# Optimization experiments

Measured on AMD Instinct MI355X. Metric: run time of the kernel, lower is better.

## Reference

```python
import jax, jax.numpy as jnp
import numpy as np

P = 0.8
XINT_MAX = 0.125; ROT_MAX = 10.0
BRI_STD = 0.2; CON_STD = 0.2; HUE_MAX = 0.95; SAT_STD = 0.2; SHARP_STD = 1.0; NOISE_STD = 0.1

def _gate(key, B, p):
    k1, k2 = jax.random.split(key)
    bern = jax.random.randint(k1, (B,), 0, 2).astype(jnp.float32)
    u = jax.random.uniform(k2, ())
    return bern * p > u  # [B] bool, matches randint(0,2)*flag*p > random()

def _sel(m, new, old):
    return jnp.where(m[:, None, None, None], new, old)

def _warp(imgs, angle_deg, tx, ty, nearest=False):
    # inverse-affine resample: rotate by angle (deg, CCW) about center, then translate (tx,ty) px; zero fill
    B, C, H, W = imgs.shape
    th = jnp.deg2rad(jnp.asarray(angle_deg, jnp.float32))
    c, s = jnp.cos(th), jnp.sin(th)
    cy, cx = (H - 1) / 2.0, (W - 1) / 2.0
    ys, xs = jnp.meshgrid(jnp.arange(H, dtype=jnp.float32), jnp.arange(W, dtype=jnp.float32), indexing='ij')
    dx = xs - cx - tx; dy = ys - cy - ty
    sx = c * dx + s * dy + cx
    sy = -s * dx + c * dy + cy
    if nearest:
        xi = jnp.round(sx); yi = jnp.round(sy)
        valid = (xi >= 0) & (xi < W) & (yi >= 0) & (yi < H)
        xc = jnp.clip(xi, 0, W - 1).astype(jnp.int32)
        yc = jnp.clip(yi, 0, H - 1).astype(jnp.int32)
        return imgs[:, :, yc, xc] * valid
    x0 = jnp.floor(sx); y0 = jnp.floor(sy)
    wx = sx - x0; wy = sy - y0
    def g(yi, xi):
        valid = (xi >= 0) & (xi < W) & (yi >= 0) & (yi < H)
        yc = jnp.clip(yi, 0, H - 1).astype(jnp.int32)
        xc = jnp.clip(xi, 0, W - 1).astype(jnp.int32)
        return imgs[:, :, yc, xc] * valid
    v00 = g(y0, x0); v01 = g(y0, x0 + 1); v10 = g(y0 + 1, x0); v11 = g(y0 + 1, x0 + 1)
    top = v00 * (1 - wx) + v01 * wx
    bot = v10 * (1 - wx) + v11 * wx
    return top * (1 - wy) + bot * wy

def _gray(x):
    return 0.2989 * x[:, 0:1] + 0.587 * x[:, 1:2] + 0.114 * x[:, 2:3]

def _blend(a, b, ratio):
    return jnp.clip(ratio * a + (1.0 - ratio) * b, 0.0, 1.0)

def _rgb_to_hsv(x):
    r, g, b = x[:, 0], x[:, 1], x[:, 2]
    maxc = jnp.maximum(jnp.maximum(r, g), b)
    minc = jnp.minimum(jnp.minimum(r, g), b)
    cr = maxc - minc
    s = cr / jnp.where(maxc == 0, 1.0, maxc)
    crd = jnp.where(cr == 0, 1.0, cr)
    rc = (maxc - r) / crd; gc = (maxc - g) / crd; bc = (maxc - b) / crd
    h = jnp.where(maxc == r, bc - gc, jnp.where(maxc == g, 2.0 + rc - bc, 4.0 + gc - rc))
    h = jnp.where(cr == 0, 0.0, (h / 6.0) % 1.0)
    return jnp.stack([h, s, maxc], axis=1)

def _hsv_to_rgb(x):
    h, s, v = x[:, 0], x[:, 1], x[:, 2]
    i = jnp.floor(h * 6.0)
    f = h * 6.0 - i
    p = v * (1 - s); q = v * (1 - f * s); t = v * (1 - (1 - f) * s)
    ii = i.astype(jnp.int32) % 6
    conds = [ii == 0, ii == 1, ii == 2, ii == 3, ii == 4, ii == 5]
    r = jnp.select(conds, [v, q, p, p, t, v])
    g = jnp.select(conds, [t, v, v, q, p, p])
    b = jnp.select(conds, [p, p, t, v, v, q])
    return jnp.stack([r, g, b], axis=1)

def _sharp_degenerate(x):
    C, H, W = x.shape[1], x.shape[2], x.shape[3]
    k = jnp.array([[1., 1., 1.], [1., 5., 1.], [1., 1., 1.]], jnp.float32) / 13.0
    w = jnp.tile(k[None, None], (C, 1, 1, 1))
    blur = jax.lax.conv_general_dilated(x, w, (1, 1), 'SAME', feature_group_count=C,
                                        dimension_numbers=('NCHW', 'OIHW', 'NCHW'))
    blur = jnp.clip(blur, 0.0, 1.0)
    interior = jnp.zeros((H, W), bool).at[1:-1, 1:-1].set(True)
    return jnp.where(interior, blur, x)  # torchvision keeps original border pixels

def _augment(images, masks):
    key = jax.random.key(42)
    ks = jax.random.split(key, 18)
    B = images.shape[0]
    img = (images + 1.0) * 0.5
    msk = masks
    # xflip
    m = _gate(ks[0], B, P)
    img = _sel(m, img[:, :, :, ::-1], img)
    msk = _sel(m, msk[:, :, :, ::-1], msk)
    # rotate90 (square images: exact)
    m = _gate(ks[1], B, P)
    img = _sel(m, jnp.rot90(img, 1, axes=(2, 3)), img)
    msk = _sel(m, jnp.rot90(msk, 1, axes=(2, 3)), msk)
    # xint translation
    m = _gate(ks[2], B, P)
    t = jax.random.uniform(ks[3], ()) * XINT_MAX
    img = _sel(m, _warp(img, 0.0, t, t), img)
    msk = _sel(m, _warp(msk, 0.0, t, t, nearest=True), msk)
    # rotate
    m = _gate(ks[4], B, P)
    r = jax.random.uniform(ks[5], ()) * ROT_MAX
    img = _sel(m, _warp(img, r, 0.0, 0.0), img)
    msk = _sel(m, _warp(msk, r, 0.0, 0.0, nearest=True), msk)
    # hue
    m = _gate(ks[6], B, P)
    h = (jax.random.uniform(ks[7], ()) - 0.5) * HUE_MAX
    hsv = _rgb_to_hsv(jnp.clip(img, 0.0, 1.0))
    hsv = hsv.at[:, 0].set((hsv[:, 0] + h) % 1.0)
    img = _sel(m, _hsv_to_rgb(hsv), img)
    # brightness
    m = _gate(ks[8], B, P)
    b = jnp.abs(1.0 + jax.random.normal(ks[9], ()) * BRI_STD)
    img = _sel(m, jnp.clip(img * b, 0.0, 1.0), img)
    # contrast
    m = _gate(ks[10], B, P)
    c = jnp.abs(1.0 + jax.random.normal(ks[11], ()) * CON_STD)
    mean = _gray(img).mean(axis=(2, 3), keepdims=True)
    img = _sel(m, _blend(img, mean, c), img)
    # saturation
    m = _gate(ks[12], B, P)
    s = jnp.abs(1.0 + jax.random.normal(ks[13], ()) * SAT_STD)
    img = _sel(m, _blend(img, _gray(img), s), img)
    # sharpness (bug-faithful: std == self.sharpness == 1.0)
    m = _gate(ks[14], B, P)
    sh = jnp.abs(1.0 + jax.random.normal(ks[15], ()) * SHARP_STD)
    img = _sel(m, _blend(img, _sharp_degenerate(img), sh), img)
    # noise
    m = _gate(ks[16], B, P)
    n = jax.random.normal(ks[17], img.shape, img.dtype) * NOISE_STD
    img = _sel(m, img + n, img)
    img = (img - 0.5) / 0.5
    return img, msk

def setup_inputs() -> dict:
    key = jax.random.key(0)
    k1, k2 = jax.random.split(key)
    images = jax.random.uniform(k1, (32, 3, 512, 512), jnp.float32, -1.0, 1.0)
    masks = (jax.random.uniform(k2, (32, 1, 512, 512), jnp.float32) > 0.5).astype(jnp.float32)
    return {"images": images, "masks": masks}

def reference(images, masks):
    return _augment(images, masks)
```

## Files before the change

### kernel.cpp

```cpp
#include <hip/hip_runtime.h>
#include <stdint.h>
#include <math.h>

#define HH 512
#define WW 512
#define BB 32
#define CC 3
#define HWSZ (HH*WW)
#define CHW (CC*HWSZ)
#define NIMG (BB*CHW)
#define NMSK (BB*HWSZ)

__host__ __device__ inline uint32_t rotl32(uint32_t x, uint32_t r){ return (x<<r)|(x>>(32u-r)); }

__host__ __device__ inline void tf2x32(uint32_t k0, uint32_t k1, uint32_t x0, uint32_t x1,
                                       uint32_t& o0, uint32_t& o1){
  uint32_t kx = k0 ^ k1 ^ 0x1BD11BDAu;
  uint32_t ks[3] = {k0, k1, kx};
  const uint32_t R[2][4] = {{13u,15u,26u,6u},{17u,29u,16u,24u}};
  x0 += ks[0]; x1 += ks[1];
  #pragma unroll
  for (int i = 0; i < 5; ++i){
    #pragma unroll
    for (int j = 0; j < 4; ++j){
      x0 += x1; x1 = rotl32(x1, R[i & 1][j]); x1 ^= x0;
    }
    x0 += ks[(i+1)%3];
    x1 += ks[(i+2)%3] + (uint32_t)(i+1);
  }
  o0 = x0; o1 = x1;
}

__host__ __device__ inline float bits_to_u01(uint32_t b){
  uint32_t fb = (b >> 9) | 0x3f800000u;
  float f;
#ifdef __HIP_DEVICE_COMPILE__
  f = __uint_as_float(fb);
#else
  union { uint32_t u; float f; } cv; cv.u = fb; f = cv.f;
#endif
  return f - 1.0f;
}

__host__ __device__ inline float erfinv_f32(float x){
  float w = -log1pf(-x*x);
  float p;
  if (w < 5.0f){
    w -= 2.5f;
    p = 2.81022636e-08f;
    p = fmaf(p, w, 3.43273939e-07f);
    p = fmaf(p, w, -3.5233877e-06f);
    p = fmaf(p, w, -4.39150654e-06f);
    p = fmaf(p, w, 0.00021858087f);
    p = fmaf(p, w, -0.00125372503f);
    p = fmaf(p, w, -0.00417768164f);
    p = fmaf(p, w, 0.246640727f);
    p = fmaf(p, w, 1.50140941f);
  } else {
    w = sqrtf(w) - 3.0f;
    p = -0.000200214257f;
    p = fmaf(p, w, 0.000100950558f);
    p = fmaf(p, w, 0.00134934322f);
    p = fmaf(p, w, -0.00367342844f);
    p = fmaf(p, w, 0.00573950773f);
    p = fmaf(p, w, -0.0076224613f);
    p = fmaf(p, w, 0.00943887047f);
    p = fmaf(p, w, 1.00167406f);
    p = fmaf(p, w, 2.83297682f);
  }
  return p * x;
}

#define NRM_LO (-0.9999999403953552f)
#define SQRT2F 1.41421356237309504880f

__host__ __device__ inline float normal_from_bits(uint32_t b){
  float f = bits_to_u01(b);
  float val = f * 2.0f + NRM_LO;
  val = fmaxf(NRM_LO, val);
  return SQRT2F * erfinv_f32(val);
}

struct Key { uint32_t a, b; };

static Key foldSplit(Key k, uint32_t j){
  Key r; tf2x32(k.a, k.b, 0u, j, r.a, r.b); return r;
}

static uint32_t bits32(Key k, uint32_t i){
  uint32_t o0, o1; tf2x32(k.a, k.b, 0u, i, o0, o1); return o0 ^ o1;
}

static float unif_scalar(Key k){ return bits_to_u01(bits32(k, 0u)); }
static float normal_scalar(Key k){ return normal_from_bits(bits32(k, 0u)); }

static uint32_t gate_mask(Key kg){
  Key k1 = foldSplit(kg, 0u);
  Key k2 = foldSplit(kg, 1u);
  Key kl = foldSplit(k1, 1u);
  float u = bits_to_u01(bits32(k2, 0u));
  uint32_t m = 0;
  for (uint32_t i = 0; i < 32; ++i){
    float bern = (float)(bits32(kl, i) & 1u);
    if (bern * 0.8f > u) m |= (1u << i);
  }
  return m;
}

struct AugParams {
  uint32_t mFlip, mRot90, mTrans, mRot, mHue, mBri, mCon, mSat, mSharp, mNoise;
  float t, rotC, rotS, hShift, bri, con, sat, shp;
  uint32_t nk0, nk1;
};

__device__ inline float clip01(float v){ return fminf(fmaxf(v, 0.0f), 1.0f); }

__device__ inline void permIdx(int y, int x, bool r9, bool fl, int& py, int& px){
  if (r9){ py = x; px = 511 - y; } else { py = y; px = x; }
  if (fl) px = 511 - px;
}

__device__ inline float tapP(const float* __restrict__ src, int y, int x, bool r9, bool fl){
  if ((unsigned)x >= 512u || (unsigned)y >= 512u) return 0.0f;
  int py, px; permIdx(y, x, r9, fl, py, px);
  return (src[py*512 + px] + 1.0f) * 0.5f;
}

__device__ inline void stage1RGB(const float* __restrict__ base, int ty, int tx,
                                 bool r9, bool fl, bool tr, float t, float out[3]){
  if (!tr){
    #pragma unroll
    for (int c = 0; c < 3; ++c) out[c] = tapP(base + c*HWSZ, ty, tx, r9, fl);
    return;
  }
  float sx = (((float)tx - 255.5f) - t) + 255.5f;
  float sy = (((float)ty - 255.5f) - t) + 255.5f;
  float x0f = floorf(sx), y0f = floorf(sy);
  float wx = sx - x0f, wy = sy - y0f;
  int x0 = (int)x0f, y0 = (int)y0f;
  #pragma unroll
  for (int c = 0; c < 3; ++c){
    const float* s = base + c*HWSZ;
    float v00 = tapP(s, y0,   x0,   r9, fl);
    float v01 = tapP(s, y0,   x0+1, r9, fl);
    float v10 = tapP(s, y0+1, x0,   r9, fl);
    float v11 = tapP(s, y0+1, x0+1, r9, fl);
    float top = v00*(1.0f-wx) + v01*wx;
    float bot = v10*(1.0f-wx) + v11*wx;
    out[c] = top*(1.0f-wy) + bot*wy;
  }
}

__device__ inline void rotTap(const float* __restrict__ base, int ty, int tx,
                              bool r9, bool fl, bool tr, float t, float o[3]){
  if ((unsigned)tx < 512u && (unsigned)ty < 512u){
    stage1RGB(base, ty, tx, r9, fl, tr, t, o);
  } else {
    o[0] = o[1] = o[2] = 0.0f;
  }
}

__device__ inline void rgb2hsv(float r, float g, float b, float& h, float& s, float& v){
  float maxc = fmaxf(fmaxf(r, g), b);
  float minc = fminf(fminf(r, g), b);
  float cr = maxc - minc;
  s = cr / ((maxc == 0.0f) ? 1.0f : maxc);
  float crd = (cr == 0.0f) ? 1.0f : cr;
  float rc = (maxc - r) / crd;
  float gc = (maxc - g) / crd;
  float bc = (maxc - b) / crd;
  float hh;
  if (maxc == r)      hh = bc - gc;
  else if (maxc == g) hh = 2.0f + rc - bc;
  else                hh = 4.0f + gc - rc;
  if (cr == 0.0f) hh = 0.0f;
  else { hh = hh / 6.0f; hh = hh - floorf(hh); }
  h = hh; v = maxc;
}

__device__ inline void hsv2rgb(float h, float s, float v, float& r, float& g, float& b){
  float i = floorf(h * 6.0f);
  float f = h * 6.0f - i;
  float p = v * (1.0f - s);
  float q = v * (1.0f - f * s);
  float t = v * (1.0f - (1.0f - f) * s);
  int ii = ((int)i) % 6;
  switch (ii){
    case 0: r = v; g = t; b = p; break;
    case 1: r = q; g = v; b = p; break;
    case 2: r = p; g = v; b = t; break;
    case 3: r = p; g = q; b = v; break;
    case 4: r = t; g = p; b = v; break;
    default: r = v; g = p; b = q; break;
  }
}

__device__ inline void applyHB(float v[3], bool hue, bool bri, const AugParams& P){
  if (hue){
    float r = clip01(v[0]), g = clip01(v[1]), bb = clip01(v[2]);
    float h, s, val;
    rgb2hsv(r, g, bb, h, s, val);
    h = h + P.hShift;
    h = h - floorf(h);
    hsv2rgb(h, s, val, v[0], v[1], v[2]);
  }
  if (bri){
    #pragma unroll
    for (int c = 0; c < 3; ++c) v[c] = clip01(v[c] * P.bri);
  }
}

__device__ inline void stage2RGB(const float* __restrict__ base, int yy, int xx,
                                 const AugParams& P, int b, float v[3]){
  bool fl  = (P.mFlip  >> b) & 1u;
  bool r9  = (P.mRot90 >> b) & 1u;
  bool tr  = (P.mTrans >> b) & 1u;
  bool rot = (P.mRot   >> b) & 1u;
  if (rot){
    float dx = (float)xx - 255.5f;
    float dy = (float)yy - 255.5f;
    float sx = (P.rotC*dx + P.rotS*dy) + 255.5f;
    float sy = (-P.rotS*dx + P.rotC*dy) + 255.5f;
    float x0f = floorf(sx), y0f = floorf(sy);
    float wx = sx - x0f, wy = sy - y0f;
    int x0 = (int)x0f, y0 = (int)y0f;
    float q00[3], q01[3], q10[3], q11[3];
    rotTap(base, y0,   x0,   r9, fl, tr, P.t, q00);
    rotTap(base, y0,   x0+1, r9, fl, tr, P.t, q01);
    rotTap(base, y0+1, x0,   r9, fl, tr, P.t, q10);
    rotTap(base, y0+1, x0+1, r9, fl, tr, P.t, q11);
    #pragma unroll
    for (int c = 0; c < 3; ++c){
      float top = q00[c]*(1.0f-wx) + q01[c]*wx;
      float bot = q10[c]*(1.0f-wx) + q11[c]*wx;
      v[c] = top*(1.0f-wy) + bot*wy;
    }
  } else {
    stage1RGB(base, yy, xx, r9, fl, tr, P.t, v);
  }
  applyHB(v, (P.mHue >> b) & 1u, (P.mBri >> b) & 1u, P);
}

__device__ inline float s1at(const float* __restrict__ s, int y, int x){
  return ((unsigned)x < 512u && (unsigned)y < 512u) ? s[y*512 + x] : 0.0f;
}

__device__ inline void stage2S1(const float* __restrict__ s1b, int yy, int xx,
                                const AugParams& P, int b, float v[3]){
  bool rot = (P.mRot >> b) & 1u;
  bool hue = (P.mHue >> b) & 1u;
  bool bri = (P.mBri >> b) & 1u;
  if (rot){
    float dx = (float)xx - 255.5f;
    float dy = (float)yy - 255.5f;
    float sx = (P.rotC*dx + P.rotS*dy) + 255.5f;
    float sy = (-P.rotS*dx + P.rotC*dy) + 255.5f;
    float x0f = floorf(sx), y0f = floorf(sy);
    float wx = sx - x0f, wy = sy - y0f;
    int x0 = (int)x0f, y0 = (int)y0f;
    #pragma unroll
    for (int c = 0; c < 3; ++c){
      const float* s = s1b + c*HWSZ;
      float v00 = s1at(s, y0,   x0);
      float v01 = s1at(s, y0,   x0+1);
      float v10 = s1at(s, y0+1, x0);
      float v11 = s1at(s, y0+1, x0+1);
      float top = v00*(1.0f-wx) + v01*wx;
      float bot = v10*(1.0f-wx) + v11*wx;
      v[c] = top*(1.0f-wy) + bot*wy;
    }
  } else {
    #pragma unroll
    for (int c = 0; c < 3; ++c) v[c] = s1b[c*HWSZ + yy*512 + xx];
  }
  applyHB(v, hue, bri, P);
}

__device__ inline void procCS(float v[3], bool con, float cmul, float cadd, bool sat, float smul){
  if (con){
    #pragma unroll
    for (int c = 0; c < 3; ++c) v[c] = clip01(cmul * v[c] + cadd);
  }
  if (sat){
    float g = 0.2989f*v[0] + 0.587f*v[1] + 0.114f*v[2];
    float gadd = (1.0f - smul) * g;
    #pragma unroll
    for (int c = 0; c < 3; ++c) v[c] = clip01(smul * v[c] + gadd);
  }
}


__global__ void kZero(float* meanAcc){
  int t = threadIdx.x;
  if (t < 32) meanAcc[t] = 0.0f;
}


__global__ __launch_bounds__(256) void kStage1(const float* __restrict__ img,
                                               float* __restrict__ S1,
                                               float* __restrict__ meanAcc, AugParams P){
  __shared__ float ptile[3][33][33];
  __shared__ float wsum[4];
  int b = blockIdx.z;
  bool fl  = (P.mFlip  >> b) & 1u;
  bool r9  = (P.mRot90 >> b) & 1u;
  bool tr  = (P.mTrans >> b) & 1u;
  bool rot = (P.mRot   >> b) & 1u;
  bool con = (P.mCon   >> b) & 1u;
  bool hue = (P.mHue   >> b) & 1u;
  bool bri = (P.mBri   >> b) & 1u;
  bool accM = con && !rot;
  int X0 = blockIdx.x*32, Y0 = blockIdx.y*32;
  int tx = threadIdx.x, ty = threadIdx.y;
  int tid = ty*32 + tx;
  const float* base = img + (size_t)b*CHW;
  float* dstb = S1 + (size_t)b*CHW;
  float t = P.t;
  float gsum = 0.0f;

  if (!r9 && !tr){
    #pragma unroll
    for (int k = 0; k < 4; ++k){
      int y = Y0 + ty + 8*k, x = X0 + tx;
      int px = fl ? (511 - x) : x;
      float v[3];
      #pragma unroll
      for (int c = 0; c < 3; ++c){
        v[c] = (base[c*HWSZ + y*512 + px] + 1.0f) * 0.5f;
        dstb[(size_t)c*HWSZ + (size_t)y*512 + x] = v[c];
      }
      if (accM){
        float w[3] = {v[0], v[1], v[2]};
        applyHB(w, hue, bri, P);
        gsum += 0.2989f*w[0] + 0.587f*w[1] + 0.114f*w[2];
      }
    }
  } else if (!r9){
    #pragma unroll
    for (int k = 0; k < 4; ++k){
      int y = Y0 + ty + 8*k, x = X0 + tx;
      float v[3];
      stage1RGB(base, y, x, false, fl, true, t, v);
      #pragma unroll
      for (int c = 0; c < 3; ++c)
        dstb[(size_t)c*HWSZ + (size_t)y*512 + x] = v[c];
      if (accM){
        float w[3] = {v[0], v[1], v[2]};
        applyHB(w, hue, bri, P);
        gsum += 0.2989f*w[0] + 0.587f*w[1] + 0.114f*w[2];
      }
    }
  } else {
    #pragma unroll
    for (int c = 0; c < 3; ++c){
      const float* src = base + c*HWSZ;
      for (int idx = tid; idx < 33*33; idx += 256){
        int r = idx / 33, q = idx - r*33;
        int xx = X0 - 1 + r;
        int yy = Y0 - 1 + q;
        float val = 0.0f;
        if ((unsigned)yy < 512u && (unsigned)xx < 512u){
          int col = fl ? yy : (511 - yy);
          val = (src[xx*512 + col] + 1.0f) * 0.5f;
        }
        ptile[c][q][r] = val;
      }
    }
    __syncthreads();
    #pragma unroll
    for (int k = 0; k < 4; ++k){
      int y = Y0 + ty + 8*k, x = X0 + tx;
      float v[3];
      if (tr){
        float sx = (((float)x - 255.5f) - t) + 255.5f;
        float sy = (((float)y - 255.5f) - t) + 255.5f;
        float x0f = floorf(sx), y0f = floorf(sy);
        float wx = sx - x0f, wy = sy - y0f;
        int lx0 = (int)x0f - (X0 - 1);
        int ly0 = (int)y0f - (Y0 - 1);
        #pragma unroll
        for (int c = 0; c < 3; ++c){
          float v00 = ptile[c][ly0][lx0],   v01 = ptile[c][ly0][lx0+1];
          float v10 = ptile[c][ly0+1][lx0], v11 = ptile[c][ly0+1][lx0+1];
          float top = v00*(1.0f-wx) + v01*wx;
          float bot = v10*(1.0f-wx) + v11*wx;
          v[c] = top*(1.0f-wy) + bot*wy;
        }
      } else {
        #pragma unroll
        for (int c = 0; c < 3; ++c) v[c] = ptile[c][ty+8*k+1][tx+1];
      }
      #pragma unroll
      for (int c = 0; c < 3; ++c)
        dstb[(size_t)c*HWSZ + (size_t)y*512 + x] = v[c];
      if (accM){
        float w[3] = {v[0], v[1], v[2]};
        applyHB(w, hue, bri, P);
        gsum += 0.2989f*w[0] + 0.587f*w[1] + 0.114f*w[2];
      }
    }
  }

  if (accM){
    #pragma unroll
    for (int off = 32; off > 0; off >>= 1) gsum += __shfl_down(gsum, off);
    int wid = tid >> 6, lid = tid & 63;
    if (lid == 0) wsum[wid] = gsum;
    __syncthreads();
    if (tid == 0) atomicAdd(&meanAcc[b], wsum[0] + wsum[1] + wsum[2] + wsum[3]);
  }
}

__global__ __launch_bounds__(256) void kMaskStage(const float* __restrict__ msk,
                                                  float* __restrict__ M1,
                                                  float* __restrict__ outMsk, AugParams P){
  __shared__ float mtile[32][33];
  int b = blockIdx.z;
  bool fl  = (P.mFlip  >> b) & 1u;
  bool r9  = (P.mRot90 >> b) & 1u;
  bool rot = (P.mRot   >> b) & 1u;
  int X0 = blockIdx.x*32, Y0 = blockIdx.y*32;
  int tx = threadIdx.x, ty = threadIdx.y;
  int tid = ty*32 + tx;
  const float* src = msk + (size_t)b*HWSZ;
  float* dst = (rot ? M1 : outMsk) + (size_t)b*HWSZ;
  if (!r9){
    #pragma unroll
    for (int k = 0; k < 4; ++k){
      int y = Y0 + ty + 8*k, x = X0 + tx;
      int px = fl ? (511 - x) : x;
      dst[y*512 + x] = src[y*512 + px];
    }
  } else {
    for (int idx = tid; idx < 32*32; idx += 256){
      int r = idx >> 5, q = idx & 31;
      int xx = X0 + r;
      int yy = Y0 + q;
      int col = fl ? yy : (511 - yy);
      mtile[q][r] = src[xx*512 + col];
    }
    __syncthreads();
    #pragma unroll
    for (int k = 0; k < 4; ++k){
      int y = Y0 + ty + 8*k, x = X0 + tx;
      dst[y*512 + x] = mtile[ty + 8*k][tx];
    }
  }
}

__global__ __launch_bounds__(256) void kMaskRot(const float* __restrict__ M1,
                                                float* __restrict__ outMsk, AugParams P){
  int b = blockIdx.z;
  if (!((P.mRot >> b) & 1u)) return;
  int X0 = blockIdx.x*32, Y0 = blockIdx.y*32;
  int tx = threadIdx.x, ty = threadIdx.y;
  const float* src = M1 + (size_t)b*HWSZ;
  float* dst = outMsk + (size_t)b*HWSZ;
  #pragma unroll
  for (int k = 0; k < 4; ++k){
    int x = X0 + tx, y = Y0 + ty + 8*k;
    float dx = __fsub_rn((float)x, 255.5f);
    float dy = __fsub_rn((float)y, 255.5f);
    float sx = __fadd_rn(__fadd_rn(__fmul_rn(P.rotC, dx), __fmul_rn(P.rotS, dy)), 255.5f);
    float sy = __fadd_rn(__fadd_rn(__fmul_rn(-P.rotS, dx), __fmul_rn(P.rotC, dy)), 255.5f);
    float xi = rintf(sx), yi = rintf(sy);
    bool valid = (xi >= 0.0f) && (xi < 512.0f) && (yi >= 0.0f) && (yi < 512.0f);
    int xc = (int)fminf(fmaxf(xi, 0.0f), 511.0f);
    int yc = (int)fminf(fmaxf(yi, 0.0f), 511.0f);
    float v = valid ? src[yc*512 + xc] : 0.0f;
    dst[y*512 + x] = v;
  }
}

__global__ __launch_bounds__(256) void kMean2(const float* __restrict__ S1,
                                              float* __restrict__ meanAcc, AugParams P){
  int b = blockIdx.z;
  if (!((P.mCon >> b) & 1u) || !((P.mRot >> b) & 1u)) return;
  int tid = threadIdx.x;
  const float* base = S1 + (size_t)b*CHW;
  int pbase = blockIdx.x * 4096;
  float lsum = 0.0f;

  #pragma unroll 4
  for (int j = 0; j < 16; ++j){
    int px = pbase + j*256 + tid;
    int y = px >> 9, x = px & 511;
    float v[3];
    stage2S1(base, y, x, P, b, v);
    lsum += 0.2989f*v[0] + 0.587f*v[1] + 0.114f*v[2];
  }

  #pragma unroll
  for (int off = 32; off > 0; off >>= 1) lsum += __shfl_down(lsum, off);
  __shared__ float wsum[4];
  int wid = tid >> 6, lid = tid & 63;
  if (lid == 0) wsum[wid] = lsum;
  __syncthreads();
  if (tid == 0) atomicAdd(&meanAcc[b], wsum[0] + wsum[1] + wsum[2] + wsum[3]);
}

__global__ __launch_bounds__(256) void kFinal2(const float* __restrict__ S1,
                                               const float* __restrict__ meanAcc,
                                               float* __restrict__ out, AugParams P){
  __shared__ float s2[34][34][3];
  int tx = threadIdx.x, ty = threadIdx.y;
  int tid = ty*32 + tx;
  int bx = blockIdx.x, by = blockIdx.y, b = blockIdx.z;
  const float W1 = 1.0f/13.0f, W5 = 5.0f/13.0f;

  bool con = (P.mCon   >> b) & 1u;
  bool sat = (P.mSat   >> b) & 1u;
  bool shg = (P.mSharp >> b) & 1u;
  bool noi = (P.mNoise >> b) & 1u;
  float mean = meanAcc[b] * (1.0f/262144.0f);
  float cadd = (1.0f - P.con) * mean;
  const float* base = S1 + (size_t)b*CHW;

  if (!shg){
    #pragma unroll
    for (int k = 0; k < 4; ++k){
      int x = bx*32 + tx, y = by*32 + ty + 8*k;
      float res[3];
      stage2S1(base, y, x, P, b, res);
      procCS(res, con, P.con, cadd, sat, P.sat);
      if (noi){
        #pragma unroll
        for (int c = 0; c < 3; ++c){
          uint32_t idx = (uint32_t)(b*CHW + c*HWSZ + y*512 + x);
          uint32_t o0, o1;
          tf2x32(P.nk0, P.nk1, 0u, idx, o0, o1);
          res[c] += normal_from_bits(o0 ^ o1) * 0.1f;
        }
      }
      #pragma unroll
      for (int c = 0; c < 3; ++c){
        out[(size_t)b*CHW + (size_t)c*HWSZ + (size_t)y*512 + x] = (res[c] - 0.5f) * 2.0f;
      }
    }
    return;
  }

  for (int cell = tid; cell < 34*34; cell += 256){
    int r = cell / 34, cc = cell - r*34;
    int gy = by*32 + r - 1, gx = bx*32 + cc - 1;
    float v[3] = {0.0f, 0.0f, 0.0f};
    if ((unsigned)gx < 512u && (unsigned)gy < 512u){
      stage2S1(base, gy, gx, P, b, v);
      procCS(v, con, P.con, cadd, sat, P.sat);
    }
    s2[r][cc][0] = v[0]; s2[r][cc][1] = v[1]; s2[r][cc][2] = v[2];
  }
  __syncthreads();

  for (int k = 0; k < 4; ++k){
    int yy = ty + 8*k;
    int x = bx*32 + tx, y = by*32 + yy;
    bool interior = (x >= 1) && (x <= 510) && (y >= 1) && (y <= 510);
    float res[3];
    float c0[3] = { s2[yy+1][tx+1][0], s2[yy+1][tx+1][1], s2[yy+1][tx+1][2] };
    if (interior){
      float nsum[3] = {0.0f, 0.0f, 0.0f};
      #pragma unroll
      for (int dy = 0; dy < 3; ++dy){
        #pragma unroll
        for (int dxx = 0; dxx < 3; ++dxx){
          if (dxx == 1 && dy == 1) continue;
          #pragma unroll
          for (int c = 0; c < 3; ++c) nsum[c] += s2[yy+dy][tx+dxx][c];
        }
      }
      #pragma unroll
      for (int c = 0; c < 3; ++c){
        float bl = clip01(nsum[c]*W1 + c0[c]*W5);
        res[c] = clip01(P.shp * c0[c] + (1.0f - P.shp) * bl);
      }
    } else {
      res[0] = c0[0]; res[1] = c0[1]; res[2] = c0[2];
    }

    if (noi){
      #pragma unroll
      for (int c = 0; c < 3; ++c){
        uint32_t idx = (uint32_t)(b*CHW + c*HWSZ + y*512 + x);
        uint32_t o0, o1;
        tf2x32(P.nk0, P.nk1, 0u, idx, o0, o1);
        res[c] += normal_from_bits(o0 ^ o1) * 0.1f;
      }
    }
    #pragma unroll
    for (int c = 0; c < 3; ++c){
      out[(size_t)b*CHW + (size_t)c*HWSZ + (size_t)y*512 + x] = (res[c] - 0.5f) * 2.0f;
    }
  }
}


__global__ __launch_bounds__(256) void kMask(const float* __restrict__ msk,
                                             float* __restrict__ out, AugParams P){
  int x = blockIdx.x*blockDim.x + threadIdx.x;
  int y = blockIdx.y*blockDim.y + threadIdx.y;
  int b = blockIdx.z;
  bool fl  = (P.mFlip  >> b) & 1u;
  bool r9  = (P.mRot90 >> b) & 1u;
  bool rot = (P.mRot   >> b) & 1u;
  float v;
  if (rot){
    float dx = __fsub_rn((float)x, 255.5f);
    float dy = __fsub_rn((float)y, 255.5f);
    float sx = __fadd_rn(__fadd_rn(__fmul_rn(P.rotC, dx), __fmul_rn(P.rotS, dy)), 255.5f);
    float sy = __fadd_rn(__fadd_rn(__fmul_rn(-P.rotS, dx), __fmul_rn(P.rotC, dy)), 255.5f);
    float xi = rintf(sx), yi = rintf(sy);
    bool valid = (xi >= 0.0f) && (xi < 512.0f) && (yi >= 0.0f) && (yi < 512.0f);
    int xc = (int)fminf(fmaxf(xi, 0.0f), 511.0f);
    int yc = (int)fminf(fmaxf(yi, 0.0f), 511.0f);
    int py, px; permIdx(yc, xc, r9, fl, py, px);
    v = valid ? msk[(size_t)b*HWSZ + py*512 + px] : 0.0f;
  } else {
    int py, px; permIdx(y, x, r9, fl, py, px);
    v = msk[(size_t)b*HWSZ + py*512 + px];
  }
  out[(size_t)b*HWSZ + y*512 + x] = v;
}

__global__ __launch_bounds__(256) void kMean(const float* __restrict__ img,
                                             float* __restrict__ meanAcc, AugParams P){
  int b = blockIdx.z;
  if (!((P.mCon >> b) & 1u)) return;
  int x = blockIdx.x*blockDim.x + threadIdx.x;
  int y = blockIdx.y*blockDim.y + threadIdx.y;
  float v[3];
  stage2RGB(img + (size_t)b*CHW, y, x, P, b, v);
  float gray = 0.2989f*v[0] + 0.587f*v[1] + 0.114f*v[2];
  __shared__ float sred[256];
  int tid = threadIdx.y*blockDim.x + threadIdx.x;
  sred[tid] = gray;
  __syncthreads();
  for (int s = 128; s > 0; s >>= 1){
    if (tid < s) sred[tid] += sred[tid + s];
    __syncthreads();
  }
  if (tid == 0) atomicAdd(&meanAcc[b], sred[0]);
}

__global__ __launch_bounds__(256) void kFinal(const float* __restrict__ img,
                                              const float* __restrict__ meanAcc,
                                              float* __restrict__ out, AugParams P){
  __shared__ float s2[10][34][3];
  int tx = threadIdx.x, ty = threadIdx.y;
  int tid = ty*32 + tx;
  int bx = blockIdx.x, by = blockIdx.y, b = blockIdx.z;
  const float W1 = 1.0f/13.0f, W5 = 5.0f/13.0f;

  bool con = (P.mCon   >> b) & 1u;
  bool sat = (P.mSat   >> b) & 1u;
  bool shg = (P.mSharp >> b) & 1u;
  bool noi = (P.mNoise >> b) & 1u;
  float mean = meanAcc[b] * (1.0f/262144.0f);
  float cadd = (1.0f - P.con) * mean;
  const float* base = img + (size_t)b*CHW;

  for (int cell = tid; cell < 340; cell += 256){
    int r = cell / 34, cc = cell % 34;
    int gy = by*8 + r - 1, gx = bx*32 + cc - 1;
    float v[3] = {0.0f, 0.0f, 0.0f};
    if ((unsigned)gx < 512u && (unsigned)gy < 512u){
      stage2RGB(base, gy, gx, P, b, v);
      procCS(v, con, P.con, cadd, sat, P.sat);
    }
    s2[r][cc][0] = v[0]; s2[r][cc][1] = v[1]; s2[r][cc][2] = v[2];
  }
  __syncthreads();

  int x = bx*32 + tx, y = by*8 + ty;
  bool interior = (x >= 1) && (x <= 510) && (y >= 1) && (y <= 510);
  float res[3];
  float c0[3] = { s2[ty+1][tx+1][0], s2[ty+1][tx+1][1], s2[ty+1][tx+1][2] };
  if (shg && interior){
    float nsum[3] = {0.0f, 0.0f, 0.0f};
    #pragma unroll
    for (int dy = 0; dy < 3; ++dy){
      #pragma unroll
      for (int dxx = 0; dxx < 3; ++dxx){
        if (dxx == 1 && dy == 1) continue;
        #pragma unroll
        for (int c = 0; c < 3; ++c) nsum[c] += s2[ty+dy][tx+dxx][c];
      }
    }
    #pragma unroll
    for (int c = 0; c < 3; ++c){
      float bl = clip01(nsum[c]*W1 + c0[c]*W5);
      res[c] = clip01(P.shp * c0[c] + (1.0f - P.shp) * bl);
    }
  } else {
    res[0] = c0[0]; res[1] = c0[1]; res[2] = c0[2];
  }

  if (noi){
    #pragma unroll
    for (int c = 0; c < 3; ++c){
      uint32_t idx = (uint32_t)(b*CHW + c*HWSZ + y*512 + x);
      uint32_t o0, o1;
      tf2x32(P.nk0, P.nk1, 0u, idx, o0, o1);
      res[c] += normal_from_bits(o0 ^ o1) * 0.1f;
    }
  }
  #pragma unroll
  for (int c = 0; c < 3; ++c){
    out[(size_t)b*CHW + (size_t)c*HWSZ + y*512 + x] = (res[c] - 0.5f) * 2.0f;
  }
}

extern "C" void kernel_launch(void* const* d_in, const int* in_sizes, int n_in,
                              void* d_out, int out_size, void* d_ws, size_t ws_size,
                              hipStream_t stream) {
  (void)in_sizes; (void)n_in; (void)out_size;
  const float* images = (const float*)d_in[0];
  const float* masks  = (const float*)d_in[1];
  float* out_img = (float*)d_out;
  float* out_msk = out_img + (size_t)NIMG;
  float* meanAcc = (float*)d_ws;

  Key root; root.a = 0u; root.b = 42u;
  Key ks[18];
  for (uint32_t j = 0; j < 18; ++j) ks[j] = foldSplit(root, j);

  AugParams P;
  P.mFlip  = gate_mask(ks[0]);
  P.mRot90 = gate_mask(ks[1]);
  P.mTrans = gate_mask(ks[2]);
  P.t      = unif_scalar(ks[3]) * 0.125f;
  P.mRot   = gate_mask(ks[4]);
  float r  = unif_scalar(ks[5]) * 10.0f;
  P.mHue   = gate_mask(ks[6]);
  P.hShift = (unif_scalar(ks[7]) - 0.5f) * 0.95f;
  P.mBri   = gate_mask(ks[8]);
  P.bri    = fabsf(1.0f + normal_scalar(ks[9])  * 0.2f);
  P.mCon   = gate_mask(ks[10]);
  P.con    = fabsf(1.0f + normal_scalar(ks[11]) * 0.2f);
  P.mSat   = gate_mask(ks[12]);
  P.sat    = fabsf(1.0f + normal_scalar(ks[13]) * 0.2f);
  P.mSharp = gate_mask(ks[14]);
  P.shp    = fabsf(1.0f + normal_scalar(ks[15]) * 1.0f);
  P.mNoise = gate_mask(ks[16]);
  P.nk0 = ks[17].a; P.nk1 = ks[17].b;

  if (!(P.t > 0.0f)) P.mTrans = 0u;

  float th = r * 0.017453292519943295f;
  P.rotC = (float)cos((double)th);
  P.rotS = (float)sin((double)th);

  dim3 blk(32, 8, 1);
  const size_t needFull = ((size_t)NIMG + (size_t)NMSK + 64) * sizeof(float);
  const size_t needImg  = ((size_t)NIMG + 64) * sizeof(float);

  kZero<<<1, 64, 0, stream>>>(meanAcc);

  if (ws_size >= needFull){
    float* S1 = (float*)d_ws + 64;
    float* M1 = S1 + (size_t)NIMG;
    kMaskStage<<<dim3(16, 16, 32), blk, 0, stream>>>(masks, M1, out_msk, P);
    kMaskRot  <<<dim3(16, 16, 32), blk, 0, stream>>>(M1, out_msk, P);
    kStage1   <<<dim3(16, 16, 32), blk, 0, stream>>>(images, S1, meanAcc, P);
    kMean2    <<<dim3(64, 1, 32), dim3(256,1,1), 0, stream>>>(S1, meanAcc, P);
    kFinal2   <<<dim3(16, 16, 32), blk, 0, stream>>>(S1, meanAcc, out_img, P);
  } else if (ws_size >= needImg){
    float* S1 = (float*)d_ws + 64;
    kMask     <<<dim3(16, 64, 32), blk, 0, stream>>>(masks, out_msk, P);
    kStage1   <<<dim3(16, 16, 32), blk, 0, stream>>>(images, S1, meanAcc, P);
    kMean2    <<<dim3(64, 1, 32), dim3(256,1,1), 0, stream>>>(S1, meanAcc, P);
    kFinal2   <<<dim3(16, 16, 32), blk, 0, stream>>>(S1, meanAcc, out_img, P);
  } else {
    kMask <<<dim3(16, 64, 32), blk, 0, stream>>>(masks, out_msk, P);
    kMean <<<dim3(16, 64, 32), blk, 0, stream>>>(images, meanAcc, P);
    kFinal<<<dim3(16, 64, 32), blk, 0, stream>>>(images, meanAcc, out_img, P);
  }
}
```

Baseline: 374.6 us.

## Fuse mask kernels into image kernels, vectorize copies, add fast final path

Merges the mask copy and mask-rotation kernels into the image stage-1 and final kernels by doubling the z grid, with extra z-slices handling the masks. This removes two launches and lets the mask work overlap the image work. The identity and flip copy paths now use float4 loads and stores. The final kernel gets a vectorized fast path for images with neither sharpness nor rotation. The HSV conversions become branchless selects, and the zeroing kernel is replaced with hipMemsetAsync. Mask blocks in the merged grids may leave SIMDs idle, and blocks that return early for mask slices still cost scheduling.

```diff
diff --git a/kernel.cpp b/kernel.cpp
--- a/kernel.cpp
+++ b/kernel.cpp
@@ -169,13 +169,11 @@
   float rc = (maxc - r) / crd;
   float gc = (maxc - g) / crd;
   float bc = (maxc - b) / crd;
-  float hh;
-  if (maxc == r)      hh = bc - gc;
-  else if (maxc == g) hh = 2.0f + rc - bc;
-  else                hh = 4.0f + gc - rc;
-  if (cr == 0.0f) hh = 0.0f;
-  else { hh = hh / 6.0f; hh = hh - floorf(hh); }
-  h = hh; v = maxc;
+  float hh = (maxc == r) ? (bc - gc) : ((maxc == g) ? (2.0f + rc - bc) : (4.0f + gc - rc));
+  float hd = hh / 6.0f;
+  hd = hd - floorf(hd);
+  h = (cr == 0.0f) ? 0.0f : hd;
+  v = maxc;
 }
 
 __device__ inline void hsv2rgb(float h, float s, float v, float& r, float& g, float& b){
@@ -185,14 +183,9 @@
   float q = v * (1.0f - f * s);
   float t = v * (1.0f - (1.0f - f) * s);
   int ii = ((int)i) % 6;
-  switch (ii){
-    case 0: r = v; g = t; b = p; break;
-    case 1: r = q; g = v; b = p; break;
-    case 2: r = p; g = v; b = t; break;
-    case 3: r = p; g = q; b = v; break;
-    case 4: r = t; g = p; b = v; break;
-    default: r = v; g = p; b = q; break;
-  }
+  r = (ii == 0 || ii == 5) ? v : (ii == 1) ? q : (ii == 4) ? t : p;
+  g = (ii == 0) ? t : (ii <= 2) ? v : (ii == 3) ? q : p;
+  b = (ii <= 1) ? p : (ii == 2) ? t : (ii <= 4) ? v : q;
 }
 
 __device__ inline void applyHB(float v[3], bool hue, bool bri, const AugParams& P){
@@ -290,18 +283,58 @@
 }
 
 
-__global__ void kZero(float* meanAcc){
-  int t = threadIdx.x;
-  if (t < 32) meanAcc[t] = 0.0f;
-}
-
-
-__global__ __launch_bounds__(256) void kStage1(const float* __restrict__ img,
-                                               float* __restrict__ S1,
-                                               float* __restrict__ meanAcc, AugParams P){
+
+__global__ __launch_bounds__(256) void kStage1M(const float* __restrict__ img,
+                                                const float* __restrict__ msk,
+                                                float* __restrict__ S1,
+                                                float* __restrict__ M1,
+                                                float* __restrict__ outMsk,
+                                                float* __restrict__ meanAcc, AugParams P){
   __shared__ float ptile[3][33][33];
   __shared__ float wsum[4];
-  int b = blockIdx.z;
+  int zz = blockIdx.z;
+  int tx = threadIdx.x, ty = threadIdx.y;
+  int tid = ty*32 + tx;
+  int X0 = blockIdx.x*32, Y0 = blockIdx.y*32;
+
+  if (zz >= BB){
+    int b = zz - BB;
+    bool fl  = (P.mFlip  >> b) & 1u;
+    bool r9  = (P.mRot90 >> b) & 1u;
+    bool rot = (P.mRot   >> b) & 1u;
+    const float* src = msk + (size_t)b*HWSZ;
+    float* dst = (rot ? M1 : outMsk) + (size_t)b*HWSZ;
+    if (!r9){
+      int row = tid >> 3, q = tid & 7;
+      int y = Y0 + row, x4 = X0 + q*4;
+      float4 u;
+      if (!fl){
+        u = *(const float4*)(src + y*512 + x4);
+      } else {
+        float4 w = *(const float4*)(src + y*512 + (508 - x4));
+        u = make_float4(w.w, w.z, w.y, w.x);
+      }
+      *(float4*)(dst + y*512 + x4) = u;
+    } else {
+      float (*mtile)[33] = reinterpret_cast<float(*)[33]>(&ptile[0][0][0]);
+      for (int idx = tid; idx < 32*32; idx += 256){
+        int r = idx >> 5, q = idx & 31;
+        int xx = X0 + r;
+        int yy = Y0 + q;
+        int col = fl ? yy : (511 - yy);
+        mtile[q][r] = src[xx*512 + col];
+      }
+      __syncthreads();
+      #pragma unroll
+      for (int k = 0; k < 4; ++k){
+        int y = Y0 + ty + 8*k, x = X0 + tx;
+        dst[y*512 + x] = mtile[ty + 8*k][tx];
+      }
+    }
+    return;
+  }
+
+  int b = zz;
   bool fl  = (P.mFlip  >> b) & 1u;
   bool r9  = (P.mRot90 >> b) & 1u;
   bool tr  = (P.mTrans >> b) & 1u;
@@ -310,27 +343,33 @@
   bool hue = (P.mHue   >> b) & 1u;
   bool bri = (P.mBri   >> b) & 1u;
   bool accM = con && !rot;
-  int X0 = blockIdx.x*32, Y0 = blockIdx.y*32;
-  int tx = threadIdx.x, ty = threadIdx.y;
-  int tid = ty*32 + tx;
   const float* base = img + (size_t)b*CHW;
   float* dstb = S1 + (size_t)b*CHW;
   float t = P.t;
   float gsum = 0.0f;
 
   if (!r9 && !tr){
-    #pragma unroll
-    for (int k = 0; k < 4; ++k){
-      int y = Y0 + ty + 8*k, x = X0 + tx;
-      int px = fl ? (511 - x) : x;
-      float v[3];
-      #pragma unroll
-      for (int c = 0; c < 3; ++c){
-        v[c] = (base[c*HWSZ + y*512 + px] + 1.0f) * 0.5f;
-        dstb[(size_t)c*HWSZ + (size_t)y*512 + x] = v[c];
-      }
-      if (accM){
-        float w[3] = {v[0], v[1], v[2]};
+    int row = tid >> 3, q = tid & 7;
+    int y = Y0 + row, x4 = X0 + q*4;
+    float vv[3][4];
+    #pragma unroll
+    for (int c = 0; c < 3; ++c){
+      float4 u;
+      if (!fl){
+        u = *(const float4*)(base + c*HWSZ + y*512 + x4);
+      } else {
+        float4 w = *(const float4*)(base + c*HWSZ + y*512 + (508 - x4));
+        u = make_float4(w.w, w.z, w.y, w.x);
+      }
+      u.x = (u.x + 1.0f)*0.5f; u.y = (u.y + 1.0f)*0.5f;
+      u.z = (u.z + 1.0f)*0.5f; u.w = (u.w + 1.0f)*0.5f;
+      *(float4*)(dstb + c*HWSZ + y*512 + x4) = u;
+      vv[c][0] = u.x; vv[c][1] = u.y; vv[c][2] = u.z; vv[c][3] = u.w;
+    }
+    if (accM){
+      #pragma unroll
+      for (int e = 0; e < 4; ++e){
+        float w[3] = {vv[0][e], vv[1][e], vv[2][e]};
         applyHB(w, hue, bri, P);
         gsum += 0.2989f*w[0] + 0.587f*w[1] + 0.114f*w[2];
       }
@@ -411,67 +450,6 @@
   }
 }
 
-__global__ __launch_bounds__(256) void kMaskStage(const float* __restrict__ msk,
-                                                  float* __restrict__ M1,
-                                                  float* __restrict__ outMsk, AugParams P){
-  __shared__ float mtile[32][33];
-  int b = blockIdx.z;
-  bool fl  = (P.mFlip  >> b) & 1u;
-  bool r9  = (P.mRot90 >> b) & 1u;
-  bool rot = (P.mRot   >> b) & 1u;
-  int X0 = blockIdx.x*32, Y0 = blockIdx.y*32;
-  int tx = threadIdx.x, ty = threadIdx.y;
-  int tid = ty*32 + tx;
-  const float* src = msk + (size_t)b*HWSZ;
-  float* dst = (rot ? M1 : outMsk) + (size_t)b*HWSZ;
-  if (!r9){
-    #pragma unroll
-    for (int k = 0; k < 4; ++k){
-      int y = Y0 + ty + 8*k, x = X0 + tx;
-      int px = fl ? (511 - x) : x;
-      dst[y*512 + x] = src[y*512 + px];
-    }
-  } else {
-    for (int idx = tid; idx < 32*32; idx += 256){
-      int r = idx >> 5, q = idx & 31;
-      int xx = X0 + r;
-      int yy = Y0 + q;
-      int col = fl ? yy : (511 - yy);
-      mtile[q][r] = src[xx*512 + col];
-    }
-    __syncthreads();
-    #pragma unroll
-    for (int k = 0; k < 4; ++k){
-      int y = Y0 + ty + 8*k, x = X0 + tx;
-      dst[y*512 + x] = mtile[ty + 8*k][tx];
-    }
-  }
-}
-
-__global__ __launch_bounds__(256) void kMaskRot(const float* __restrict__ M1,
-                                                float* __restrict__ outMsk, AugParams P){
-  int b = blockIdx.z;
-  if (!((P.mRot >> b) & 1u)) return;
-  int X0 = blockIdx.x*32, Y0 = blockIdx.y*32;
-  int tx = threadIdx.x, ty = threadIdx.y;
-  const float* src = M1 + (size_t)b*HWSZ;
-  float* dst = outMsk + (size_t)b*HWSZ;
-  #pragma unroll
-  for (int k = 0; k < 4; ++k){
-    int x = X0 + tx, y = Y0 + ty + 8*k;
-    float dx = __fsub_rn((float)x, 255.5f);
-    float dy = __fsub_rn((float)y, 255.5f);
-    float sx = __fadd_rn(__fadd_rn(__fmul_rn(P.rotC, dx), __fmul_rn(P.rotS, dy)), 255.5f);
-    float sy = __fadd_rn(__fadd_rn(__fmul_rn(-P.rotS, dx), __fmul_rn(P.rotC, dy)), 255.5f);
-    float xi = rintf(sx), yi = rintf(sy);
-    bool valid = (xi >= 0.0f) && (xi < 512.0f) && (yi >= 0.0f) && (yi < 512.0f);
-    int xc = (int)fminf(fmaxf(xi, 0.0f), 511.0f);
-    int yc = (int)fminf(fmaxf(yi, 0.0f), 511.0f);
-    float v = valid ? src[yc*512 + xc] : 0.0f;
-    dst[y*512 + x] = v;
-  }
-}
-
 __global__ __launch_bounds__(256) void kMean2(const float* __restrict__ S1,
                                               float* __restrict__ meanAcc, AugParams P){
   int b = blockIdx.z;
@@ -499,15 +477,45 @@
   if (tid == 0) atomicAdd(&meanAcc[b], wsum[0] + wsum[1] + wsum[2] + wsum[3]);
 }
 
-__global__ __launch_bounds__(256) void kFinal2(const float* __restrict__ S1,
+__global__ __launch_bounds__(256) void kFinalM(const float* __restrict__ S1,
+                                               const float* __restrict__ M1,
                                                const float* __restrict__ meanAcc,
-                                               float* __restrict__ out, AugParams P){
+                                               float* __restrict__ out,
+                                               float* __restrict__ outMsk, AugParams P){
   __shared__ float s2[34][34][3];
+  int zz = blockIdx.z;
   int tx = threadIdx.x, ty = threadIdx.y;
   int tid = ty*32 + tx;
-  int bx = blockIdx.x, by = blockIdx.y, b = blockIdx.z;
+  int bx = blockIdx.x, by = blockIdx.y;
+
+  if (zz >= BB){
+    int b = zz - BB;
+    if (!((P.mRot >> b) & 1u)) return;
+    const float* src = M1 + (size_t)b*HWSZ;
+    float* dst = outMsk + (size_t)b*HWSZ;
+    int X0 = bx*32, Y0 = by*32;
+    #pragma unroll
+    for (int k = 0; k < 4; ++k){
+      int x = X0 + tx, y = Y0 + ty + 8*k;
+      float dx = __fsub_rn((float)x, 255.5f);
+      float dy = __fsub_rn((float)y, 255.5f);
+      float sx = __fadd_rn(__fadd_rn(__fmul_rn(P.rotC, dx), __fmul_rn(P.rotS, dy)), 255.5f);
+      float sy = __fadd_rn(__fadd_rn(__fmul_rn(-P.rotS, dx), __fmul_rn(P.rotC, dy)), 255.5f);
+      float xi = rintf(sx), yi = rintf(sy);
+      bool valid = (xi >= 0.0f) && (xi < 512.0f) && (yi >= 0.0f) && (yi < 512.0f);
+      int xc = (int)fminf(fmaxf(xi, 0.0f), 511.0f);
+      int yc = (int)fminf(fmaxf(yi, 0.0f), 511.0f);
+      float v = valid ? src[yc*512 + xc] : 0.0f;
+      dst[y*512 + x] = v;
+    }
+    return;
+  }
+
+  int b = zz;
   const float W1 = 1.0f/13.0f, W5 = 5.0f/13.0f;
-
+  bool rot = (P.mRot   >> b) & 1u;
+  bool hue = (P.mHue   >> b) & 1u;
+  bool bri = (P.mBri   >> b) & 1u;
   bool con = (P.mCon   >> b) & 1u;
   bool sat = (P.mSat   >> b) & 1u;
   bool shg = (P.mSharp >> b) & 1u;
@@ -515,6 +523,41 @@
   float mean = meanAcc[b] * (1.0f/262144.0f);
   float cadd = (1.0f - P.con) * mean;
   const float* base = S1 + (size_t)b*CHW;
+
+  if (!shg && !rot){
+    int row = tid >> 3, q = tid & 7;
+    int y = by*32 + row; int x4 = bx*32 + q*4;
+    float4 rv = *(const float4*)(base + y*512 + x4);
+    float4 gv = *(const float4*)(base + HWSZ + y*512 + x4);
+    float4 bv = *(const float4*)(base + 2*HWSZ + y*512 + x4);
+    float R[4] = {rv.x, rv.y, rv.z, rv.w};
+    float G[4] = {gv.x, gv.y, gv.z, gv.w};
+    float B[4] = {bv.x, bv.y, bv.z, bv.w};
+    float O[3][4];
+    #pragma unroll
+    for (int e = 0; e < 4; ++e){
+      float v[3] = {R[e], G[e], B[e]};
+      applyHB(v, hue, bri, P);
+      procCS(v, con, P.con, cadd, sat, P.sat);
+      if (noi){
+        #pragma unroll
+        for (int c = 0; c < 3; ++c){
+          uint32_t idx = (uint32_t)(b*CHW + c*HWSZ + y*512 + x4 + e);
+          uint32_t o0, o1;
+          tf2x32(P.nk0, P.nk1, 0u, idx, o0, o1);
+          v[c] += normal_from_bits(o0 ^ o1) * 0.1f;
+        }
+      }
+      #pragma unroll
+      for (int c = 0; c < 3; ++c) O[c][e] = (v[c] - 0.5f) * 2.0f;
+    }
+    #pragma unroll
+    for (int c = 0; c < 3; ++c){
+      float4 w = make_float4(O[c][0], O[c][1], O[c][2], O[c][3]);
+      *(float4*)(out + (size_t)b*CHW + (size_t)c*HWSZ + (size_t)y*512 + x4) = w;
+    }
+    return;
+  }
 
   if (!shg){
     #pragma unroll
@@ -754,22 +797,20 @@
   const size_t needFull = ((size_t)NIMG + (size_t)NMSK + 64) * sizeof(float);
   const size_t needImg  = ((size_t)NIMG + 64) * sizeof(float);
 
-  kZero<<<1, 64, 0, stream>>>(meanAcc);
+  hipMemsetAsync(meanAcc, 0, 32*sizeof(float), stream);
 
   if (ws_size >= needFull){
     float* S1 = (float*)d_ws + 64;
     float* M1 = S1 + (size_t)NIMG;
-    kMaskStage<<<dim3(16, 16, 32), blk, 0, stream>>>(masks, M1, out_msk, P);
-    kMaskRot  <<<dim3(16, 16, 32), blk, 0, stream>>>(M1, out_msk, P);
-    kStage1   <<<dim3(16, 16, 32), blk, 0, stream>>>(images, S1, meanAcc, P);
-    kMean2    <<<dim3(64, 1, 32), dim3(256,1,1), 0, stream>>>(S1, meanAcc, P);
-    kFinal2   <<<dim3(16, 16, 32), blk, 0, stream>>>(S1, meanAcc, out_img, P);
+    kStage1M<<<dim3(16, 16, 64), blk, 0, stream>>>(images, masks, S1, M1, out_msk, meanAcc, P);
+    kMean2  <<<dim3(64, 1, 32), dim3(256,1,1), 0, stream>>>(S1, meanAcc, P);
+    kFinalM <<<dim3(16, 16, 64), blk, 0, stream>>>(S1, M1, meanAcc, out_img, out_msk, P);
   } else if (ws_size >= needImg){
     float* S1 = (float*)d_ws + 64;
-    kMask     <<<dim3(16, 64, 32), blk, 0, stream>>>(masks, out_msk, P);
-    kStage1   <<<dim3(16, 16, 32), blk, 0, stream>>>(images, S1, meanAcc, P);
-    kMean2    <<<dim3(64, 1, 32), dim3(256,1,1), 0, stream>>>(S1, meanAcc, P);
-    kFinal2   <<<dim3(16, 16, 32), blk, 0, stream>>>(S1, meanAcc, out_img, P);
+    kMask   <<<dim3(16, 64, 32), blk, 0, stream>>>(masks, out_msk, P);
+    kStage1M<<<dim3(16, 16, 32), blk, 0, stream>>>(images, masks, S1, nullptr, out_msk, meanAcc, P);
+    kMean2  <<<dim3(64, 1, 32), dim3(256,1,1), 0, stream>>>(S1, meanAcc, P);
+    kFinalM <<<dim3(16, 16, 32), blk, 0, stream>>>(S1, nullptr, meanAcc, out_img, out_msk, P);
   } else {
     kMask <<<dim3(16, 64, 32), blk, 0, stream>>>(masks, out_msk, P);
     kMean <<<dim3(16, 64, 32), blk, 0, stream>>>(images, meanAcc, P);
```

Result: faster. 358.6 us (-4.3%).
